# Kernel tuning notes

Hardware: AMD Instinct MI355X
Metric: run time of the kernel (lower is better)

Reference implementation:

```python
import jax, jax.numpy as jnp
import numpy as np

COMMITMENT_COST = 0.25


def setup_inputs() -> dict:
    key = jax.random.key(0)
    k1, k2 = jax.random.split(key)
    N, K, D = 131072, 1024, 64
    inputs = jax.random.normal(k1, (N, D), dtype=jnp.float32)
    # torch init: uniform(-1/K, 1/K); use randn scaled similarly-small for a generic table
    embedding = jax.random.uniform(k2, (K, D), dtype=jnp.float32,
                                   minval=-1.0 / K, maxval=1.0 / K)
    return {"inputs": inputs, "embedding": embedding}


def reference(inputs, embedding):
    distances = (jnp.sum(inputs ** 2, axis=1, keepdims=True)
                 + jnp.sum(embedding ** 2, axis=1)
                 - 2.0 * inputs @ embedding.T)
    encoding_indices = jnp.argmin(distances, axis=1)            # [N]
    # direct gather (same math as one-hot @ embedding)
    quantized = embedding[encoding_indices]                     # [N, D]

    diff2 = jnp.mean((quantized - inputs) ** 2)
    # e_latent_loss == q_latent_loss numerically in fwd
    loss = diff2 + COMMITMENT_COST * diff2

    # straight-through output (forward value == quantized)
    quantized_st = inputs + jax.lax.stop_gradient(quantized - inputs)

    # avg_probs via histogram instead of materializing [N, K] one-hot
    N, K = inputs.shape[0], embedding.shape[0]
    counts = jnp.zeros((K,), dtype=jnp.float32).at[encoding_indices].add(1.0)
    avg_probs = counts / N
    perplexity = jnp.exp(-jnp.sum(avg_probs * jnp.log(avg_probs + 1e-10)))

    return quantized_st, loss, encoding_indices.reshape(N, 1), perplexity
```

## Files before the change

### kernel.cpp

```cpp
#include <hip/hip_runtime.h>
#include <hip/hip_bf16.h>

#define D 64
#define MARGIN 8e-5f
#define KS 2
#define RB 8

typedef __attribute__((ext_vector_type(8))) short bf16x8;
typedef __attribute__((ext_vector_type(4))) float f32x4;
typedef __attribute__((ext_vector_type(4))) unsigned uint4v;


__device__ __forceinline__ float np_pairwise_sumsq64(const float* a) {
    float r[8];
#pragma unroll
    for (int j = 0; j < 8; ++j) r[j] = __fmul_rn(a[j], a[j]);
#pragma unroll
    for (int i = 8; i < 64; i += 8)
#pragma unroll
        for (int j = 0; j < 8; ++j)
            r[j] = __fadd_rn(r[j], __fmul_rn(a[i + j], a[i + j]));
    return __fadd_rn(
        __fadd_rn(__fadd_rn(r[0], r[1]), __fadd_rn(r[2], r[3])),
        __fadd_rn(__fadd_rn(r[4], r[5]), __fadd_rn(r[6], r[7])));
}

#define CVT8(F0, F1, H, L)                                                    \
    do {                                                                      \
        float _f[8] = {F0.x, F0.y, F0.z, F0.w, F1.x, F1.y, F1.z, F1.w};       \
        _Pragma("unroll") for (int _i = 0; _i < 8; ++_i) {                    \
            unsigned _u = __float_as_uint(_f[_i]);                            \
            unsigned _hb = (_u + 0x7fffu + ((_u >> 16) & 1u)) >> 16;          \
            float _hf = __uint_as_float(_hb << 16);                           \
            float _r = _f[_i] - _hf;                                          \
            unsigned _u2 = __float_as_uint(_r);                               \
            unsigned _lb = (_u2 + 0x7fffu + ((_u2 >> 16) & 1u)) >> 16;        \
            H[_i] = (short)_hb;                                               \
            L[_i] = (short)_lb;                                               \
        }                                                                     \
    } while (0)

__global__ __launch_bounds__(256) void vq_prep_all(
    const float* __restrict__ emb, int K,
    float* __restrict__ eenp, float* __restrict__ neh,
    unsigned short* __restrict__ ehs, float* __restrict__ eT,
    unsigned* __restrict__ counts, unsigned* __restrict__ done,
    unsigned* __restrict__ nunc) {
    int b = blockIdx.x;
    if (b < 64) {
        int t = b * 256 + threadIdx.x;
        int tile = t >> 8, r = t & 255, s = r >> 6, l = r & 63;
        int sub = l & 15, grp = l >> 4;
        int k = tile * 16 + sub;
        int d0 = ((s & 1) << 5) + (grp << 3);
        const float* e = emb + (size_t)k * D + d0;
        float4 f0 = *(const float4*)e;
        float4 f1 = *(const float4*)(e + 4);
        bf16x8 h, lo;
        CVT8(f0, f1, h, lo);
        *(bf16x8*)(ehs + (size_t)t * 8) = (s >> 1) ? lo : h;
    } else if (b < 68) {
        int k = (b - 64) * 256 + threadIdx.x;
        float s = np_pairwise_sumsq64(emb + (size_t)k * D);
        eenp[k] = s;
        neh[k] = -0.5f * s;
    } else if (b < 324) {
        int t = (b - 68) * 256 + threadIdx.x;
        int d = t / K, k = t - d * K;
        eT[t] = emb[(size_t)k * D + d];
    } else {
#pragma unroll
        for (int i = 0; i < 4; ++i) {
            int c = threadIdx.x + 256 * i;
            if (c < K) counts[c] = 0u;
        }
        if (threadIdx.x == 0) { *done = 0u; *nunc = 0u; }
    }
}

__global__ __launch_bounds__(256) void vq_screen(
    const float* __restrict__ x, const unsigned short* __restrict__ ehs,
    const float* __restrict__ neh, int N, int K,
    float* __restrict__ m1p, float* __restrict__ m2p, int* __restrict__ bip,
    float* __restrict__ xxp) {
    const int tid = threadIdx.x;
    const int lane = tid & 63;
    const int wid = tid >> 6;
    const int kslice = blockIdx.x & (KS - 1);
    const int rowblk = blockIdx.x >> 1;
    const int row0 = rowblk * 256 + wid * 64;
    const int sub = lane & 15, grp = lane >> 4;
    const int g4 = grp << 2;
    const int k0 = kslice * (K / KS);
    const int NT = (K / KS) >> 4;
    const int t0 = k0 >> 4;

    __shared__ __align__(16) unsigned short lds[2][2048];

    bf16x8 xh[4][2], xl[4][2];
    float xq[4];
#pragma unroll
    for (int rt = 0; rt < 4; ++rt) {
        xq[rt] = 0.f;
        const float* xrow = x + (((size_t)(row0 + (rt << 4) + sub)) << 6) + (grp << 3);
#pragma unroll
        for (int s = 0; s < 2; ++s) {
            float4 f0 = *(const float4*)(xrow + (s << 5));
            float4 f1 = *(const float4*)(xrow + (s << 5) + 4);
            xq[rt] = fmaf(f0.x, f0.x, xq[rt]); xq[rt] = fmaf(f0.y, f0.y, xq[rt]);
            xq[rt] = fmaf(f0.z, f0.z, xq[rt]); xq[rt] = fmaf(f0.w, f0.w, xq[rt]);
            xq[rt] = fmaf(f1.x, f1.x, xq[rt]); xq[rt] = fmaf(f1.y, f1.y, xq[rt]);
            xq[rt] = fmaf(f1.z, f1.z, xq[rt]); xq[rt] = fmaf(f1.w, f1.w, xq[rt]);
            CVT8(f0, f1, xh[rt][s], xl[rt][s]);
        }
    }
#pragma unroll
    for (int rt = 0; rt < 4; ++rt) {
        xq[rt] += __shfl_xor(xq[rt], 16);
        xq[rt] += __shfl_xor(xq[rt], 32);
    }

    float m1[4], m2[4];
#pragma unroll
    for (int rt = 0; rt < 4; ++rt) { m1[rt] = -3e38f; m2[rt] = -3e38f; }

    const unsigned short* sbase = ehs + ((size_t)t0 << 11);
    const int slot = (wid << 9) + (lane << 3);

    uint4v tmp = *(const uint4v*)(sbase + slot);
    *(uint4v*)&lds[0][slot] = tmp;
    __syncthreads();

    for (int t = 0; t < NT; ++t) {
        const int cur = t & 1;
        if (t + 1 < NT)
            tmp = *(const uint4v*)(sbase + ((size_t)(t + 1) << 11) + slot);

        f32x4 cb = *(const f32x4*)(neh + k0 + (t << 4) + g4);
        const bf16x8* L = (const bf16x8*)&lds[cur][0];
        bf16x8 a0 = L[lane];
        bf16x8 a1 = L[64 + lane];
        bf16x8 a2 = L[128 + lane];
        bf16x8 a3 = L[192 + lane];

        f32x4 acc[4];
#pragma unroll
        for (int rt = 0; rt < 4; ++rt)
            acc[rt] = __builtin_amdgcn_mfma_f32_16x16x32_bf16(a0, xh[rt][0], cb, 0, 0, 0);
#pragma unroll
        for (int rt = 0; rt < 4; ++rt)
            acc[rt] = __builtin_amdgcn_mfma_f32_16x16x32_bf16(a2, xh[rt][0], acc[rt], 0, 0, 0);
#pragma unroll
        for (int rt = 0; rt < 4; ++rt)
            acc[rt] = __builtin_amdgcn_mfma_f32_16x16x32_bf16(a0, xl[rt][0], acc[rt], 0, 0, 0);
#pragma unroll
        for (int rt = 0; rt < 4; ++rt)
            acc[rt] = __builtin_amdgcn_mfma_f32_16x16x32_bf16(a1, xh[rt][1], acc[rt], 0, 0, 0);
#pragma unroll
        for (int rt = 0; rt < 4; ++rt)
            acc[rt] = __builtin_amdgcn_mfma_f32_16x16x32_bf16(a3, xh[rt][1], acc[rt], 0, 0, 0);
#pragma unroll
        for (int rt = 0; rt < 4; ++rt)
            acc[rt] = __builtin_amdgcn_mfma_f32_16x16x32_bf16(a1, xl[rt][1], acc[rt], 0, 0, 0);

        const int baset = 511 - (t << 4) - g4;
#pragma unroll
        for (int rt = 0; rt < 4; ++rt) {
#pragma unroll
            for (int j = 0; j < 4; ++j) {
                unsigned pv = (__float_as_uint(acc[rt][j]) & 0xFFFFFE00u)
                              | (unsigned)(baset - j);
                float p = __uint_as_float(pv);
                m2[rt] = fminf(fmaxf(p, m2[rt]), m1[rt]);
                m1[rt] = fmaxf(p, m1[rt]);
            }
        }

        if (t + 1 < NT)
            *(uint4v*)&lds[cur ^ 1][slot] = tmp;
        __syncthreads();
    }

#pragma unroll
    for (int rt = 0; rt < 4; ++rt) {
#pragma unroll
        for (int off = 16; off <= 32; off <<= 1) {
            float om1 = __shfl_xor(m1[rt], off);
            float om2 = __shfl_xor(m2[rt], off);
            float lo = fminf(m1[rt], om1);
            m1[rt] = fmaxf(m1[rt], om1);
            m2[rt] = fmaxf(lo, fmaxf(m2[rt], om2));
        }
    }

    if (lane < 16) {
#pragma unroll
        for (int rt = 0; rt < 4; ++rt) {
            size_t idx = (size_t)kslice * N + row0 + (rt << 4) + lane;
            int local = 511 - (int)(__float_as_uint(m1[rt]) & 511u);
            m1p[idx] = m1[rt];
            m2p[idx] = m2[rt];
            bip[idx] = k0 + local;
            if (kslice == 0) xxp[row0 + (rt << 4) + lane] = xq[rt];
        }
    }
}

__global__ __launch_bounds__(256) void vq_epilogue(
    const float* __restrict__ emb,
    const float* __restrict__ m1p, const float* __restrict__ m2p,
    const int* __restrict__ bip, const float* __restrict__ xxp, int N,
    float* __restrict__ outq, float* __restrict__ outidx,
    double* __restrict__ lossA,
    unsigned* __restrict__ nunc, unsigned* __restrict__ list) {
    const int tid = threadIdx.x;
    const int rows0 = blockIdx.x * 64;
    __shared__ int sdec[64];

    if (tid < 64) {
        int r = rows0 + tid;
        float gm1 = m1p[r], gm2 = m2p[r];
        int gbi = bip[r];
#pragma unroll
        for (int s = 1; s < KS; ++s) {
            size_t idx = (size_t)s * N + r;
            float m1b = m1p[idx], m2b = m2p[idx];
            int bb = bip[idx];
            bool take = m1b > gm1;
            float lo = fminf(gm1, m1b);
            gm1 = fmaxf(gm1, m1b);
            gm2 = fmaxf(lo, fmaxf(gm2, m2b));
            gbi = take ? bb : gbi;
        }
        bool amb = 2.0f * (gm1 - gm2) < MARGIN;
        unsigned long long mask = __ballot(amb);
        int cnt = __popcll(mask);
        unsigned base = 0;
        if (tid == 0 && cnt) base = atomicAdd(nunc, (unsigned)cnt);
        base = __shfl(base, 0);
        int dec = gbi;
        double lpart = 0.0;
        if (amb) {
            int rank = __popcll(mask & ((1ull << tid) - 1ull));
            list[base + rank] = (unsigned)r;
            dec = -1;
        } else {
            outidx[r] = (float)dec;
            float gm1v = __uint_as_float(__float_as_uint(gm1) & 0xFFFFFE00u);
            lpart = (double)(xxp[r] - 2.0f * gm1v);
        }
        sdec[tid] = dec;
#pragma unroll
        for (int off = 32; off; off >>= 1) lpart += __shfl_down(lpart, off);
        if (tid == 0) lossA[blockIdx.x] = lpart;
    }
    __syncthreads();

    const int chunk = tid & 15, rl = tid >> 4;
#pragma unroll
    for (int p = 0; p < 4; ++p) {
        int lr = p * 16 + rl;
        int dp = sdec[lr];
        if (dp >= 0) {
            float4 ev = *(const float4*)(emb + (size_t)dp * D + chunk * 4);
            *(float4*)(outq + (size_t)(rows0 + lr) * D + chunk * 4) = ev;
        }
    }
}

__global__ __launch_bounds__(256) void vq_resolve(
    const float* __restrict__ x, const float* __restrict__ emb,
    const float* __restrict__ eT, const float* __restrict__ eenp,
    int N, int K,
    float* __restrict__ outq, float* __restrict__ outidx,
    double* __restrict__ lossR,
    const unsigned* __restrict__ nunc, const unsigned* __restrict__ list) {
    const unsigned n = *nunc;
    const int tid = threadIdx.x;
    const int w = tid >> 6, l = tid & 63;
    const f32x4* eT4 = (const f32x4*)eT;
    __shared__ float sxr[RB][64];
    __shared__ float sxx[RB];
    __shared__ float swm[RB][4];
    __shared__ int swi[RB][4];
    __shared__ int sres[RB];
    double lacc = 0.0;

    for (unsigned base = blockIdx.x * RB; base < n; base += gridDim.x * RB) {
        const int nb = (int)(n - base < (unsigned)RB ? n - base : (unsigned)RB);
#pragma unroll
        for (int i = tid; i < RB * 64; i += 256) {
            int r = i >> 6, d = i & 63;
            if (r < nb) sxr[r][d] = x[(size_t)list[base + r] * D + d];
        }
        __syncthreads();
        if (tid < nb) sxx[tid] = np_pairwise_sumsq64(&sxr[tid][0]);
        __syncthreads();

        f32x4 dt[RB];
#pragma unroll
        for (int r = 0; r < RB; ++r) dt[r] = (f32x4){0.f, 0.f, 0.f, 0.f};
#pragma unroll 4
        for (int d = 0; d < D; ++d) {
            f32x4 ev = eT4[(size_t)d * 256 + tid];
#pragma unroll
            for (int r = 0; r < RB; ++r) {
                float xv = sxr[r][d];
                dt[r][0] = __fmaf_rn(xv, ev[0], dt[r][0]);
                dt[r][1] = __fmaf_rn(xv, ev[1], dt[r][1]);
                dt[r][2] = __fmaf_rn(xv, ev[2], dt[r][2]);
                dt[r][3] = __fmaf_rn(xv, ev[3], dt[r][3]);
            }
        }

#pragma unroll
        for (int r = 0; r < RB; ++r) {
            if (r >= nb) break;
            float xx = sxx[r];
            float bm = 1e30f;
            int bi = 0;
#pragma unroll
            for (int jj = 0; jj < 4; ++jj) {
                int k = (tid << 2) + jj;
                float dist = __fsub_rn(__fadd_rn(xx, eenp[k]),
                                       __fmul_rn(2.0f, dt[r][jj]));
                if (dist < bm) { bm = dist; bi = k; }
            }
#pragma unroll
            for (int off = 1; off < 64; off <<= 1) {
                float ov = __shfl_xor(bm, off);
                int oi = __shfl_xor(bi, off);
                if (ov < bm || (ov == bm && oi < bi)) { bm = ov; bi = oi; }
            }
            if (l == 0) { swm[r][w] = bm; swi[r][w] = bi; }
        }
        __syncthreads();
        if (tid < nb) {
            float fm = swm[tid][0];
            int fi = swi[tid][0];
#pragma unroll
            for (int ww = 1; ww < 4; ++ww) {
                float ov = swm[tid][ww];
                int oi = swi[tid][ww];
                if (ov < fm || (ov == fm && oi < fi)) { fm = ov; fi = oi; }
            }
            sres[tid] = fi;
            outidx[list[base + tid]] = (float)fi;
            lacc += (double)fm;
        }
        __syncthreads();
        for (int i = tid; i < RB * 64; i += 256) {
            int r = i >> 6, d = i & 63;
            if (r < nb)
                outq[(size_t)list[base + r] * D + d] =
                    emb[(size_t)sres[r] * D + d];
        }
        __syncthreads();
    }
#pragma unroll
    for (int off = 32; off; off >>= 1) lacc += __shfl_down(lacc, off);
    __shared__ double lsw;
    if (tid == 0) lsw = lacc;
    __syncthreads();
    if (tid == 0) lossR[blockIdx.x] = lsw;
}

__global__ __launch_bounds__(256) void vq_histperp(
    const float* __restrict__ outidx, int N, int K,
    unsigned* __restrict__ counts, unsigned* __restrict__ done,
    const double* __restrict__ lossA, int nA,
    const double* __restrict__ lossR, int nR,
    float* __restrict__ out_loss, float* __restrict__ out_perp) {
    __shared__ unsigned h[1024];
    __shared__ unsigned rank_s;
#pragma unroll
    for (int i = 0; i < 4; ++i) h[threadIdx.x + 256 * i] = 0;
    __syncthreads();
    int per = N / gridDim.x;
    int base = blockIdx.x * per;
    for (int i = threadIdx.x; i < per; i += 256) {
        int k = (int)outidx[base + i];
        atomicAdd(&h[k], 1u);
    }
    __syncthreads();
#pragma unroll
    for (int i = 0; i < 4; ++i) {
        int b = threadIdx.x + 256 * i;
        unsigned v = h[b];
        if (b < K && v) atomicAdd(counts + b, v);
    }
    __threadfence();
    if (threadIdx.x == 0) rank_s = atomicAdd(done, 1u);
    __syncthreads();
    if (rank_s == gridDim.x - 1) {
        double part = 0.0;
        for (int k = threadIdx.x; k < K; k += 256) {
            unsigned c = atomicAdd(counts + k, 0u);
            double p = (double)c / (double)N;
            part += p * log(p + 1e-10);
        }
        double lsum = 0.0;
        for (int i = threadIdx.x; i < nA; i += 256) lsum += lossA[i];
        for (int i = threadIdx.x; i < nR; i += 256) lsum += lossR[i];
#pragma unroll
        for (int off = 32; off; off >>= 1) {
            part += __shfl_down(part, off);
            lsum += __shfl_down(lsum, off);
        }
        __shared__ double ls[4], ls2[4];
        if ((threadIdx.x & 63) == 0) {
            ls[threadIdx.x >> 6] = part;
            ls2[threadIdx.x >> 6] = lsum;
        }
        __syncthreads();
        if (threadIdx.x == 0) {
            double s = ls[0] + ls[1] + ls[2] + ls[3];
            double L = ls2[0] + ls2[1] + ls2[2] + ls2[3];
            *out_perp = (float)exp(-s);
            *out_loss = (float)(1.25 * (L / ((double)N * (double)D)));
        }
    }
}

extern "C" void kernel_launch(void* const* d_in, const int* in_sizes, int n_in,
                              void* d_out, int out_size, void* d_ws, size_t ws_size,
                              hipStream_t stream) {
    const float* x = (const float*)d_in[0];
    const float* emb = (const float*)d_in[1];
    int N = in_sizes[0] / D;
    int K = in_sizes[1] / D;

    float* outq = (float*)d_out;
    float* out_loss = outq + (size_t)N * D;
    float* outidx = out_loss + 1;
    float* out_perp = outidx + N;

    char* ws = (char*)d_ws;
    unsigned* counts = (unsigned*)ws;
    unsigned* done = (unsigned*)(ws + (size_t)K * 4);
    unsigned* nunc = (unsigned*)(ws + (size_t)K * 4 + 4);
    size_t off = (size_t)K * 4 + 16;
    float* neh = (float*)(ws + off);            off += (size_t)K * 4;
    float* eenp = (float*)(ws + off);           off += (size_t)K * 4;
    unsigned short* ehs = (unsigned short*)(ws + off);  off += (size_t)K * 256;
    float* eT = (float*)(ws + off);              off += (size_t)K * D * 4;
    float* m1p = (float*)(ws + off);             off += (size_t)KS * N * 4;
    float* m2p = (float*)(ws + off);             off += (size_t)KS * N * 4;
    int* bip = (int*)(ws + off);                 off += (size_t)KS * N * 4;
    float* xxp = (float*)(ws + off);             off += (size_t)N * 4;
    unsigned* list = (unsigned*)(ws + off);      off += (size_t)N * 4;
    int nA = N / 64, nR = 128;
    double* lossA = (double*)(ws + off);         off += (size_t)nA * 8;
    double* lossR = (double*)(ws + off);         off += (size_t)nR * 8;

    vq_prep_all<<<325, 256, 0, stream>>>(emb, K, eenp, neh, ehs, eT,
                                         counts, done, nunc);
    vq_screen<<<(N / 256) * KS, 256, 0, stream>>>(x, ehs, neh, N, K,
                                                  m1p, m2p, bip, xxp);
    vq_epilogue<<<N / 64, 256, 0, stream>>>(emb, m1p, m2p, bip, xxp, N,
                                            outq, outidx, lossA, nunc, list);
    vq_resolve<<<128, 256, 0, stream>>>(x, emb, eT, eenp, N, K,
                                        outq, outidx, lossR, nunc, list);
    vq_histperp<<<16, 256, 0, stream>>>(outidx, N, K, counts, done,
                                        lossA, nA, lossR, nR,
                                        out_loss, out_perp);
}
```

Before: 166.4 us.

## Fuse screen and epilogue into one 512-thread block with in-LDS K-slice merge

The screen and epilogue kernels become one kernel. Each 512-thread block covers 256 rows, with two groups of four waves each scanning half of the codebook. The per-half top-2 results are merged through shared memory instead of being written to global m1/m2/bi/xx buffers and read back by a separate kernel. This removes one launch and the global round trip of partial results, at the cost of larger blocks, more LDS per block, and fewer blocks in flight.

```diff
diff --git a/kernel.cpp b/kernel.cpp
--- a/kernel.cpp
+++ b/kernel.cpp
@@ -3,7 +3,6 @@
 
 #define D 64
 #define MARGIN 8e-5f
-#define KS 2
 #define RB 8
 
 typedef __attribute__((ext_vector_type(8))) short bf16x8;
@@ -78,24 +77,30 @@
     }
 }
 
-__global__ __launch_bounds__(256) void vq_screen(
+__global__ __launch_bounds__(512) void vq_main(
     const float* __restrict__ x, const unsigned short* __restrict__ ehs,
-    const float* __restrict__ neh, int N, int K,
-    float* __restrict__ m1p, float* __restrict__ m2p, int* __restrict__ bip,
-    float* __restrict__ xxp) {
+    const float* __restrict__ neh, const float* __restrict__ emb,
+    int N, int K,
+    float* __restrict__ outq, float* __restrict__ outidx,
+    double* __restrict__ lossA,
+    unsigned* __restrict__ nunc, unsigned* __restrict__ list) {
     const int tid = threadIdx.x;
     const int lane = tid & 63;
     const int wid = tid >> 6;
-    const int kslice = blockIdx.x & (KS - 1);
-    const int rowblk = blockIdx.x >> 1;
-    const int row0 = rowblk * 256 + wid * 64;
+    const int half = wid >> 2;
+    const int wq = wid & 3;
+    const int rows0 = blockIdx.x * 256;
+    const int row0 = rows0 + wq * 64;
     const int sub = lane & 15, grp = lane >> 4;
     const int g4 = grp << 2;
-    const int k0 = kslice * (K / KS);
-    const int NT = (K / KS) >> 4;
+    const int k0 = half * (K >> 1);
+    const int NT = (K >> 1) >> 4;
     const int t0 = k0 >> 4;
 
-    __shared__ __align__(16) unsigned short lds[2][2048];
+    __shared__ __align__(16) unsigned short lds[2][2][2048];
+    __shared__ float sm1[2][256], sm2[2][256], sxx[256];
+    __shared__ int sdec[256];
+    __shared__ double ls[4];
 
     bf16x8 xh[4][2], xl[4][2];
     float xq[4];
@@ -125,10 +130,10 @@
     for (int rt = 0; rt < 4; ++rt) { m1[rt] = -3e38f; m2[rt] = -3e38f; }
 
     const unsigned short* sbase = ehs + ((size_t)t0 << 11);
-    const int slot = (wid << 9) + (lane << 3);
+    const int slot = (wq << 9) + (lane << 3);
 
     uint4v tmp = *(const uint4v*)(sbase + slot);
-    *(uint4v*)&lds[0][slot] = tmp;
+    *(uint4v*)&lds[half][0][slot] = tmp;
     __syncthreads();
 
     for (int t = 0; t < NT; ++t) {
@@ -137,7 +142,7 @@
             tmp = *(const uint4v*)(sbase + ((size_t)(t + 1) << 11) + slot);
 
         f32x4 cb = *(const f32x4*)(neh + k0 + (t << 4) + g4);
-        const bf16x8* L = (const bf16x8*)&lds[cur][0];
+        const bf16x8* L = (const bf16x8*)&lds[half][cur][0];
         bf16x8 a0 = L[lane];
         bf16x8 a1 = L[64 + lane];
         bf16x8 a2 = L[128 + lane];
@@ -177,7 +182,7 @@
         }
 
         if (t + 1 < NT)
-            *(uint4v*)&lds[cur ^ 1][slot] = tmp;
+            *(uint4v*)&lds[half][cur ^ 1][slot] = tmp;
         __syncthreads();
     }
 
@@ -196,70 +201,54 @@
     if (lane < 16) {
 #pragma unroll
         for (int rt = 0; rt < 4; ++rt) {
-            size_t idx = (size_t)kslice * N + row0 + (rt << 4) + lane;
-            int local = 511 - (int)(__float_as_uint(m1[rt]) & 511u);
-            m1p[idx] = m1[rt];
-            m2p[idx] = m2[rt];
-            bip[idx] = k0 + local;
-            if (kslice == 0) xxp[row0 + (rt << 4) + lane] = xq[rt];
-        }
-    }
-}
-
-__global__ __launch_bounds__(256) void vq_epilogue(
-    const float* __restrict__ emb,
-    const float* __restrict__ m1p, const float* __restrict__ m2p,
-    const int* __restrict__ bip, const float* __restrict__ xxp, int N,
-    float* __restrict__ outq, float* __restrict__ outidx,
-    double* __restrict__ lossA,
-    unsigned* __restrict__ nunc, unsigned* __restrict__ list) {
-    const int tid = threadIdx.x;
-    const int rows0 = blockIdx.x * 64;
-    __shared__ int sdec[64];
-
-    if (tid < 64) {
-        int r = rows0 + tid;
-        float gm1 = m1p[r], gm2 = m2p[r];
-        int gbi = bip[r];
-#pragma unroll
-        for (int s = 1; s < KS; ++s) {
-            size_t idx = (size_t)s * N + r;
-            float m1b = m1p[idx], m2b = m2p[idx];
-            int bb = bip[idx];
-            bool take = m1b > gm1;
-            float lo = fminf(gm1, m1b);
-            gm1 = fmaxf(gm1, m1b);
-            gm2 = fmaxf(lo, fmaxf(gm2, m2b));
-            gbi = take ? bb : gbi;
-        }
+            int lr = wq * 64 + (rt << 4) + lane;
+            sm1[half][lr] = m1[rt];
+            sm2[half][lr] = m2[rt];
+            if (half == 0) sxx[lr] = xq[rt];
+        }
+    }
+    __syncthreads();
+
+    if (tid < 256) {
+        const int lr = tid;
+        const int r = rows0 + lr;
+        float m1a = sm1[0][lr], m1b = sm1[1][lr];
+        float m2a = sm2[0][lr], m2b = sm2[1][lr];
+        bool take = m1b > m1a;
+        float gm1 = fmaxf(m1a, m1b);
+        float gm2 = fmaxf(fminf(m1a, m1b), fmaxf(m2a, m2b));
+        int loc = 511 - (int)(__float_as_uint(gm1) & 511u);
+        int k = (take ? (K >> 1) : 0) + loc;
         bool amb = 2.0f * (gm1 - gm2) < MARGIN;
         unsigned long long mask = __ballot(amb);
         int cnt = __popcll(mask);
         unsigned base = 0;
-        if (tid == 0 && cnt) base = atomicAdd(nunc, (unsigned)cnt);
+        if (lane == 0 && cnt) base = atomicAdd(nunc, (unsigned)cnt);
         base = __shfl(base, 0);
-        int dec = gbi;
+        int dec = k;
         double lpart = 0.0;
         if (amb) {
-            int rank = __popcll(mask & ((1ull << tid) - 1ull));
+            int rank = __popcll(mask & ((1ull << lane) - 1ull));
             list[base + rank] = (unsigned)r;
             dec = -1;
         } else {
             outidx[r] = (float)dec;
             float gm1v = __uint_as_float(__float_as_uint(gm1) & 0xFFFFFE00u);
-            lpart = (double)(xxp[r] - 2.0f * gm1v);
-        }
-        sdec[tid] = dec;
+            lpart = (double)(sxx[lr] - 2.0f * gm1v);
+        }
+        sdec[lr] = dec;
 #pragma unroll
         for (int off = 32; off; off >>= 1) lpart += __shfl_down(lpart, off);
-        if (tid == 0) lossA[blockIdx.x] = lpart;
-    }
-    __syncthreads();
+        if (lane == 0) ls[wid] = lpart;
+    }
+    __syncthreads();
+    if (tid == 0)
+        lossA[blockIdx.x] = ls[0] + ls[1] + ls[2] + ls[3];
 
     const int chunk = tid & 15, rl = tid >> 4;
 #pragma unroll
-    for (int p = 0; p < 4; ++p) {
-        int lr = p * 16 + rl;
+    for (int p = 0; p < 8; ++p) {
+        int lr = p * 32 + rl;
         int dp = sdec[lr];
         if (dp >= 0) {
             float4 ev = *(const float4*)(emb + (size_t)dp * D + chunk * 4);
@@ -444,21 +433,15 @@
     float* eenp = (float*)(ws + off);           off += (size_t)K * 4;
     unsigned short* ehs = (unsigned short*)(ws + off);  off += (size_t)K * 256;
     float* eT = (float*)(ws + off);              off += (size_t)K * D * 4;
-    float* m1p = (float*)(ws + off);             off += (size_t)KS * N * 4;
-    float* m2p = (float*)(ws + off);             off += (size_t)KS * N * 4;
-    int* bip = (int*)(ws + off);                 off += (size_t)KS * N * 4;
-    float* xxp = (float*)(ws + off);             off += (size_t)N * 4;
     unsigned* list = (unsigned*)(ws + off);      off += (size_t)N * 4;
-    int nA = N / 64, nR = 128;
+    int nA = N / 256, nR = 128;
     double* lossA = (double*)(ws + off);         off += (size_t)nA * 8;
     double* lossR = (double*)(ws + off);         off += (size_t)nR * 8;
 
     vq_prep_all<<<325, 256, 0, stream>>>(emb, K, eenp, neh, ehs, eT,
                                          counts, done, nunc);
-    vq_screen<<<(N / 256) * KS, 256, 0, stream>>>(x, ehs, neh, N, K,
-                                                  m1p, m2p, bip, xxp);
-    vq_epilogue<<<N / 64, 256, 0, stream>>>(emb, m1p, m2p, bip, xxp, N,
-                                            outq, outidx, lossA, nunc, list);
+    vq_main<<<N / 256, 512, 0, stream>>>(x, ehs, neh, emb, N, K,
+                                         outq, outidx, lossA, nunc, list);
     vq_resolve<<<128, 256, 0, stream>>>(x, emb, eT, eenp, N, K,
                                         outq, outidx, lossR, nunc, list);
     vq_histperp<<<16, 256, 0, stream>>>(outidx, N, K, counts, done,
```

Result: no change. 165.0 us (-0.8%).
